# Performance work log

Measured on AMD Instinct MI355X. Metric: run time of the kernel, lower is better.

## Reference

```python
import jax, jax.numpy as jnp
import numpy as np

ALPHA = 0.2  # leaky relu slope
NEG = -9e15  # mask fill value from the torch code


def gat_layer(x, adj_mask, W, a):
    """One dense GAT attention head.
    Equivalent math to the torch layer, without materializing the
    [N, N, 2F] a_input tensor: a^T [h_i ; h_j] = (h @ a1)_i + (h @ a2)_j.
    x: [N, Fin], adj_mask: [N, N] bool, W: [Fin, Fout], a: [2*Fout, 1].
    """
    h = x @ W                              # [N, Fout]
    Fo = W.shape[1]
    s_src = h @ a[:Fo, 0]                  # [N]
    s_dst = h @ a[Fo:, 0]                  # [N]
    e = jax.nn.leaky_relu(s_src[:, None] + s_dst[None, :], ALPHA)  # [N, N]
    e = jnp.where(adj_mask, e, NEG)
    attn = jax.nn.softmax(e, axis=1)       # dropout is a no-op in eval mode
    return attn @ h                        # [N, Fout]


def setup_inputs() -> dict:
    key = jax.random.key(0)
    ks = jax.random.split(key, 6)
    N, nfeat, nhid, nclass, nheads = 4096, 512, 64, 32, 8
    x = jax.random.normal(ks[0], (N, nfeat), dtype=jnp.float32)
    adj = jax.random.randint(ks[1], (N, N), 0, 2, dtype=jnp.int32)
    # params scaled like torch uniform(-1/sqrt(fan_in), 1/sqrt(fan_in))
    W_att = jax.random.normal(ks[2], (nheads, nfeat, nhid), dtype=jnp.float32) / np.sqrt(nfeat)
    a_att = jax.random.normal(ks[3], (nheads, 2 * nhid, 1), dtype=jnp.float32) / np.sqrt(2 * nhid)
    W_out = jax.random.normal(ks[4], (nhid * nheads, nclass), dtype=jnp.float32) / np.sqrt(nhid * nheads)
    a_out = jax.random.normal(ks[5], (2 * nclass, 1), dtype=jnp.float32) / np.sqrt(2 * nclass)
    return {"x": x, "adj": adj, "W_att": W_att, "a_att": a_att,
            "W_out": W_out, "a_out": a_out}


def reference(x, adj, W_att, a_att, W_out, a_out):
    adj_mask = adj > 0  # [N, N]
    # multi-head layer, concat=True => elu per head, concat along features
    heads = jax.vmap(lambda W, a: jax.nn.elu(gat_layer(x, adj_mask, W, a)))(W_att, a_att)  # [H, N, nhid]
    H, N, Fh = heads.shape
    hcat = jnp.transpose(heads, (1, 0, 2)).reshape(N, H * Fh)  # [N, H*nhid]
    # output layer, concat=False, then elu applied by GAT.forward
    out = jax.nn.elu(gat_layer(hcat, adj_mask, W_out, a_out))  # [N, nclass]
    return out
```

## Files before the change

### kernel.cpp

```cpp
#include <hip/hip_runtime.h>
#include <math.h>

#define NN 4096
#define CC 512
#define MB (1024*1024)
#define LOG2E 1.4426950408889634f

typedef __attribute__((ext_vector_type(8))) __bf16 bf16x8;
typedef __attribute__((ext_vector_type(4))) float f32x4;
typedef unsigned short ushort_t;
typedef unsigned int uint_t;
typedef unsigned char uchar_t;

#if __has_builtin(__builtin_amdgcn_exp2f)
#define EXP2(x) __builtin_amdgcn_exp2f(x)
#else
#define EXP2(x) exp2f(x)
#endif

static __device__ __forceinline__ float elu1(float x){ return x > 0.f ? x : (__expf(x)-1.f); }
static __device__ __forceinline__ ushort_t f2bf(float f){
    union { float f; uint_t u; } v; v.f = f;
    uint_t r = (v.u + 0x7FFFu + ((v.u >> 16) & 1u)) >> 16;
    return (ushort_t)r;
}
static __device__ __forceinline__ float bf2f(ushort_t h){
    union { uint_t u; float f; } q; q.u = ((uint_t)h) << 16; return q.f;
}

__global__ void k_prepW(const float* __restrict__ Watt,
                        ushort_t* __restrict__ Wh, ushort_t* __restrict__ Wl){
    int idx = blockIdx.x*256 + threadIdx.x;
    int c = idx >> 7, kq = idx & 127, k = kq*4;
    ushort4 h4, l4;
    float v[4];
    #pragma unroll
    for(int j=0;j<4;j++)
        v[j] = Watt[(c>>6)*(512*64) + (k+j)*64 + (c&63)];
    h4.x = f2bf(v[0]); h4.y = f2bf(v[1]); h4.z = f2bf(v[2]); h4.w = f2bf(v[3]);
    l4.x = f2bf(v[0]-bf2f(h4.x)); l4.y = f2bf(v[1]-bf2f(h4.y));
    l4.z = f2bf(v[2]-bf2f(h4.z)); l4.w = f2bf(v[3]-bf2f(h4.w));
    *(ushort4*)&Wh[(size_t)c*512 + k] = h4;
    *(ushort4*)&Wl[(size_t)c*512 + k] = l4;
}

__global__ void k_splitx(const float* __restrict__ x,
                         ushort_t* __restrict__ xh, ushort_t* __restrict__ xl){
    int idx = blockIdx.x*256 + threadIdx.x;
    float4 v = *(const float4*)&x[(size_t)idx*4];
    ushort4 h4, l4;
    h4.x = f2bf(v.x); h4.y = f2bf(v.y); h4.z = f2bf(v.z); h4.w = f2bf(v.w);
    l4.x = f2bf(v.x-bf2f(h4.x)); l4.y = f2bf(v.y-bf2f(h4.y));
    l4.z = f2bf(v.z-bf2f(h4.z)); l4.w = f2bf(v.w-bf2f(h4.w));
    *(ushort4*)&xh[(size_t)idx*4] = h4;
    *(ushort4*)&xl[(size_t)idx*4] = l4;
}

__global__ void k_pack(const int* __restrict__ adj, uint_t* __restrict__ abits){
    int idx = blockIdx.x*256 + threadIdx.x;
    int i = idx >> 7, q = idx & 127;
    const int4* p = (const int4*)&adj[(size_t)i*NN + q*32];
    uint_t m = 0;
    #pragma unroll
    for(int g=0; g<8; g++){
        int4 v = p[g];
        m |= (uint_t)(v.x > 0) << (g*4 + 0);
        m |= (uint_t)(v.y > 0) << (g*4 + 1);
        m |= (uint_t)(v.z > 0) << (g*4 + 2);
        m |= (uint_t)(v.w > 0) << (g*4 + 3);
    }
    abits[idx] = m;
}

__global__ __launch_bounds__(256) void k_gemm1(
        const ushort_t* __restrict__ xh, const ushort_t* __restrict__ xl,
        const ushort_t* __restrict__ Wh, const ushort_t* __restrict__ Wl,
        const float* __restrict__ aatt,
        ushort_t* __restrict__ hT,
        float* __restrict__ ssrc2, float* __restrict__ sdst2){
    const int t = threadIdx.x;
    const int l = t & 63, wv = t >> 6;
    const int lr = l & 15, lg = l >> 4;
    const int ib = blockIdx.x*64 + wv*16;
    const int hd = blockIdx.y;
    const int j0 = hd*64;

    f32x4 acc[4] = {};
    #pragma unroll 2
    for(int ks=0; ks<16; ks++){
        const int kb = ks*32 + lg*8;
        bf16x8 ah = *(const bf16x8*)&xh[(size_t)(ib+lr)*512 + kb];
        bf16x8 al = *(const bf16x8*)&xl[(size_t)(ib+lr)*512 + kb];
        bf16x8 bh[4], bl[4];
        #pragma unroll
        for(int nt=0;nt<4;nt++){
            bh[nt] = *(const bf16x8*)&Wh[(size_t)(j0+nt*16+lr)*512 + kb];
            bl[nt] = *(const bf16x8*)&Wl[(size_t)(j0+nt*16+lr)*512 + kb];
        }
        #pragma unroll
        for(int nt=0;nt<4;nt++){
            acc[nt] = __builtin_amdgcn_mfma_f32_16x16x32_bf16(ah, bh[nt], acc[nt], 0,0,0);
            acc[nt] = __builtin_amdgcn_mfma_f32_16x16x32_bf16(al, bh[nt], acc[nt], 0,0,0);
            acc[nt] = __builtin_amdgcn_mfma_f32_16x16x32_bf16(ah, bl[nt], acc[nt], 0,0,0);
        }
    }
    #pragma unroll
    for(int nt=0;nt<4;nt++){
        const int col = j0 + nt*16 + lr;
        ushort4 o;
        o.x = f2bf(acc[nt][0]); o.y = f2bf(acc[nt][1]);
        o.z = f2bf(acc[nt][2]); o.w = f2bf(acc[nt][3]);
        *(ushort4*)&hT[(size_t)col*NN + ib + lg*4] = o;
    }
    float a1v[4], a2v[4];
    #pragma unroll
    for(int nt=0;nt<4;nt++){
        a1v[nt] = aatt[hd*128 + nt*16 + lr];
        a2v[nt] = aatt[hd*128 + 64 + nt*16 + lr];
    }
    #pragma unroll
    for(int r=0;r<4;r++){
        float ps = acc[0][r]*a1v[0] + acc[1][r]*a1v[1] + acc[2][r]*a1v[2] + acc[3][r]*a1v[3];
        float pd = acc[0][r]*a2v[0] + acc[1][r]*a2v[1] + acc[2][r]*a2v[2] + acc[3][r]*a2v[3];
        #pragma unroll
        for(int m=1;m<16;m<<=1){
            ps += __shfl_xor(ps, m);
            pd += __shfl_xor(pd, m);
        }
        if (lr == 0){
            ssrc2[hd*NN + ib + lg*4 + r] = ps*LOG2E;
            sdst2[hd*NN + ib + lg*4 + r] = pd*LOG2E;
        }
    }
}

__global__ __launch_bounds__(256) void k_attn1(
        const ushort_t* __restrict__ hT,
        const float* __restrict__ ssrc2, const float* __restrict__ sdst2,
        const uchar_t* __restrict__ abits,
        float* __restrict__ pnumT, float* __restrict__ pden){
    const int t = threadIdx.x;
    const int l = t & 63, wv = t >> 6;
    const int hd = blockIdx.z;
    const int i0 = blockIdx.x*64;
    const int jcc = blockIdx.y;
    const int lr = l & 15, lg = l >> 4;

    f32x4 acc[4][4] = {};
    f32x4 dacc[4] = {};

    float ss[4];
    #pragma unroll
    for(int mh=0;mh<4;mh++)
        ss[mh] = ssrc2[hd*NN + i0 + mh*16 + lr];

    bf16x8 ones;
    #pragma unroll
    for(int e=0;e<8;e++) ones[e] = (__bf16)1.0f;

    const int jwb = jcc*1024 + wv*256;
    const uchar_t* arow[4];
    #pragma unroll
    for(int mh=0;mh<4;mh++)
        arow[mh] = &abits[(size_t)(i0 + mh*16 + lr)*512 + (jwb >> 3)];

    bf16x8 bA[4], bB[4];
    float4 sdaA, sdbA, sdaB, sdbB;
    uint_t bitsA[4], bitsB[4];

#define LOAD1(SFX, JT) { \
    const int jb_ = jwb + (JT)*32 + lg*8; \
    _Pragma("unroll") \
    for(int nt=0;nt<4;nt++) \
        b##SFX[nt] = *(const bf16x8*)&hT[(size_t)(hd*64 + nt*16 + lr)*NN + jb_]; \
    sda##SFX = *(const float4*)&sdst2[hd*NN + jb_]; \
    sdb##SFX = *(const float4*)&sdst2[hd*NN + jb_ + 4]; \
    _Pragma("unroll") \
    for(int mh=0;mh<4;mh++) \
        bits##SFX[mh] = arow[mh][(JT)*4 + lg]; }

#define COMP1(SFX) { \
    float sdv[8] = {sda##SFX.x, sda##SFX.y, sda##SFX.z, sda##SFX.w, \
                    sdb##SFX.x, sdb##SFX.y, sdb##SFX.z, sdb##SFX.w}; \
    _Pragma("unroll") \
    for(int mh=0;mh<4;mh++){ \
        const uint_t bits = bits##SFX[mh]; \
        bf16x8 a; \
        _Pragma("unroll") \
        for(int e=0;e<8;e++){ \
            float s_ = ss[mh] + sdv[e]; \
            float t_ = fmaxf(s_, 0.2f*s_); \
            float w_ = EXP2(t_) * (float)((bits >> e) & 1u); \
            a[e] = (__bf16)w_; \
        } \
        _Pragma("unroll") \
        for(int nt=0;nt<4;nt++) \
            acc[mh][nt] = __builtin_amdgcn_mfma_f32_16x16x32_bf16( \
                a, b##SFX[nt], acc[mh][nt], 0, 0, 0); \
        dacc[mh] = __builtin_amdgcn_mfma_f32_16x16x32_bf16( \
                a, ones, dacc[mh], 0, 0, 0); \
    } }

    LOAD1(A, 0);
    for(int jt=0; jt<8; jt+=2){
        LOAD1(B, jt+1);
        COMP1(A);
        if (jt + 2 < 8) LOAD1(A, jt+2);
        COMP1(B);
    }
#undef LOAD1
#undef COMP1

    __shared__ f32x4 red[2][20][64];
    __syncthreads();
    if (wv >= 2){
        #pragma unroll
        for(int mh=0;mh<4;mh++){
            #pragma unroll
            for(int nt=0;nt<4;nt++) red[wv-2][mh*4+nt][l] = acc[mh][nt];
            red[wv-2][16+mh][l] = dacc[mh];
        }
    }
    __syncthreads();
    if (wv < 2){
        #pragma unroll
        for(int mh=0;mh<4;mh++){
            #pragma unroll
            for(int nt=0;nt<4;nt++) acc[mh][nt] += red[wv][mh*4+nt][l];
            dacc[mh] += red[wv][16+mh][l];
        }
    }
    __syncthreads();
    if (wv == 1){
        #pragma unroll
        for(int mh=0;mh<4;mh++){
            #pragma unroll
            for(int nt=0;nt<4;nt++) red[0][mh*4+nt][l] = acc[mh][nt];
            red[0][16+mh][l] = dacc[mh];
        }
    }
    __syncthreads();
    if (wv == 0){
        #pragma unroll
        for(int mh=0;mh<4;mh++){
            #pragma unroll
            for(int nt=0;nt<4;nt++){
                f32x4 v = acc[mh][nt] + red[0][mh*4+nt][l];
                int col = hd*64 + nt*16 + lr;
                float4 o = {v[0], v[1], v[2], v[3]};
                *(float4*)&pnumT[((size_t)jcc*512 + col)*NN + i0 + mh*16 + lg*4] = o;
            }
            f32x4 d = dacc[mh] + red[0][16+mh][l];
            if (lr == 0){
                #pragma unroll
                for(int r=0;r<4;r++)
                    pden[((size_t)jcc*8 + hd)*NN + i0 + mh*16 + lg*4 + r] = d[r];
            }
        }
    }
}

__global__ void k_reduce1T(const float* __restrict__ pnumT, const float* __restrict__ pden,
                           float* __restrict__ hcatT){
    int idx = blockIdx.x*256 + threadIdx.x;
    int c = idx >> 12, i = idx & 4095, hd = c >> 6;
    float s = 0.f, d = 0.f;
    #pragma unroll
    for(int jc=0;jc<4;jc++){
        s += pnumT[((size_t)jc*512 + c)*NN + i];
        d += pden[((size_t)jc*8 + hd)*NN + i];
    }
    hcatT[(size_t)c*NN + i] = elu1(s/d);
}

__global__ __launch_bounds__(256) void k_gemm2(const float* __restrict__ AT,
                                               const float* __restrict__ B,
                                               const float* __restrict__ aout,
                                               ushort_t* __restrict__ h2T,
                                               float* __restrict__ ss2,
                                               float* __restrict__ sd2){
    __shared__ float As[32][32];
    __shared__ float Bs[32][32];
    const int t = threadIdx.x;
    const int i0 = blockIdx.x*32;
    const int ty = t >> 4, tx = t & 15;
    float acc[2][2] = {{0.f,0.f},{0.f,0.f}};
    for(int k0=0;k0<512;k0+=32){
        __syncthreads();
        { int k = t >> 3, i4 = (t & 7)*4;
          *(float4*)&As[k][i4] = *(const float4*)&AT[(size_t)(k0+k)*NN + i0 + i4]; }
        { int k = t >> 3, n4 = (t & 7)*4;
          *(float4*)&Bs[k][n4] = *(const float4*)&B[(size_t)(k0+k)*32 + n4]; }
        __syncthreads();
        #pragma unroll
        for(int k=0;k<32;k++){
            float2 a2 = *(const float2*)&As[k][ty*2];
            float2 b2 = *(const float2*)&Bs[k][tx*2];
            acc[0][0] += a2.x*b2.x; acc[0][1] += a2.x*b2.y;
            acc[1][0] += a2.y*b2.x; acc[1][1] += a2.y*b2.y;
        }
    }
    #pragma unroll
    for(int a=0;a<2;a++){
        #pragma unroll
        for(int b=0;b<2;b++)
            h2T[(size_t)(tx*2+b)*NN + i0 + ty*2 + a] = f2bf(acc[a][b]);
    }
    float a1x = aout[tx*2], a1y = aout[tx*2+1];
    float a2x = aout[32+tx*2], a2y = aout[32+tx*2+1];
    #pragma unroll
    for(int a=0;a<2;a++){
        float ps = acc[a][0]*a1x + acc[a][1]*a1y;
        float pd = acc[a][0]*a2x + acc[a][1]*a2y;
        #pragma unroll
        for(int m=1;m<16;m<<=1){
            ps += __shfl_xor(ps, m);
            pd += __shfl_xor(pd, m);
        }
        if (tx == 0){
            ss2[i0 + ty*2 + a] = ps*LOG2E;
            sd2[i0 + ty*2 + a] = pd*LOG2E;
        }
    }
}

__global__ __launch_bounds__(256) void k_attn2(
        const ushort_t* __restrict__ h2T,
        const float* __restrict__ ss2, const float* __restrict__ sd2,
        const uchar_t* __restrict__ abits,
        float* __restrict__ pnum2T, float* __restrict__ pden2){
    const int t = threadIdx.x;
    const int l = t & 63, wv = t >> 6;
    const int i0 = blockIdx.x*64;
    const int jc = blockIdx.y;
    const int lr = l & 15, lg = l >> 4;

    f32x4 acc[4][2] = {};
    f32x4 dacc[4] = {};

    float ss[4];
    #pragma unroll
    for(int mh=0;mh<4;mh++)
        ss[mh] = ss2[i0 + mh*16 + lr];

    bf16x8 ones;
    #pragma unroll
    for(int e=0;e<8;e++) ones[e] = (__bf16)1.0f;

    const int jwb = jc*512 + wv*128;
    const uchar_t* arow[4];
    #pragma unroll
    for(int mh=0;mh<4;mh++)
        arow[mh] = &abits[(size_t)(i0 + mh*16 + lr)*512 + (jwb >> 3)];

    bf16x8 bA[2], bB[2];
    float4 sdaA, sdbA, sdaB, sdbB;
    uint_t bitsA[4], bitsB[4];

#define LOAD2(SFX, JT) { \
    const int jb_ = jwb + (JT)*32 + lg*8; \
    _Pragma("unroll") \
    for(int nt=0;nt<2;nt++) \
        b##SFX[nt] = *(const bf16x8*)&h2T[(size_t)(nt*16 + lr)*NN + jb_]; \
    sda##SFX = *(const float4*)&sd2[jb_]; \
    sdb##SFX = *(const float4*)&sd2[jb_ + 4]; \
    _Pragma("unroll") \
    for(int mh=0;mh<4;mh++) \
        bits##SFX[mh] = arow[mh][(JT)*4 + lg]; }

#define COMP2(SFX) { \
    float sdv[8] = {sda##SFX.x, sda##SFX.y, sda##SFX.z, sda##SFX.w, \
                    sdb##SFX.x, sdb##SFX.y, sdb##SFX.z, sdb##SFX.w}; \
    _Pragma("unroll") \
    for(int mh=0;mh<4;mh++){ \
        const uint_t bits = bits##SFX[mh]; \
        bf16x8 a; \
        _Pragma("unroll") \
        for(int e=0;e<8;e++){ \
            float s_ = ss[mh] + sdv[e]; \
            float t_ = fmaxf(s_, 0.2f*s_); \
            float w_ = EXP2(t_) * (float)((bits >> e) & 1u); \
            a[e] = (__bf16)w_; \
        } \
        _Pragma("unroll") \
        for(int nt=0;nt<2;nt++) \
            acc[mh][nt] = __builtin_amdgcn_mfma_f32_16x16x32_bf16( \
                a, b##SFX[nt], acc[mh][nt], 0, 0, 0); \
        dacc[mh] = __builtin_amdgcn_mfma_f32_16x16x32_bf16( \
                a, ones, dacc[mh], 0, 0, 0); \
    } }

    LOAD2(A, 0);
    for(int jt=0; jt<4; jt+=2){
        LOAD2(B, jt+1);
        COMP2(A);
        if (jt + 2 < 4) LOAD2(A, jt+2);
        COMP2(B);
    }
#undef LOAD2
#undef COMP2

    __shared__ f32x4 red2[2][12][64];
    __syncthreads();
    if (wv >= 2){
        #pragma unroll
        for(int mh=0;mh<4;mh++){
            #pragma unroll
            for(int nt=0;nt<2;nt++) red2[wv-2][mh*2+nt][l] = acc[mh][nt];
            red2[wv-2][8+mh][l] = dacc[mh];
        }
    }
    __syncthreads();
    if (wv < 2){
        #pragma unroll
        for(int mh=0;mh<4;mh++){
            #pragma unroll
            for(int nt=0;nt<2;nt++) acc[mh][nt] += red2[wv][mh*2+nt][l];
            dacc[mh] += red2[wv][8+mh][l];
        }
    }
    __syncthreads();
    if (wv == 1){
        #pragma unroll
        for(int mh=0;mh<4;mh++){
            #pragma unroll
            for(int nt=0;nt<2;nt++) red2[0][mh*2+nt][l] = acc[mh][nt];
            red2[0][8+mh][l] = dacc[mh];
        }
    }
    __syncthreads();
    if (wv == 0){
        #pragma unroll
        for(int mh=0;mh<4;mh++){
            #pragma unroll
            for(int nt=0;nt<2;nt++){
                f32x4 v = acc[mh][nt] + red2[0][mh*2+nt][l];
                int col = nt*16 + lr;
                float4 o = {v[0], v[1], v[2], v[3]};
                *(float4*)&pnum2T[((size_t)jc*32 + col)*NN + i0 + mh*16 + lg*4] = o;
            }
            f32x4 d = dacc[mh] + red2[0][8+mh][l];
            if (lr == 0){
                #pragma unroll
                for(int r=0;r<4;r++)
                    pden2[(size_t)jc*NN + i0 + mh*16 + lg*4 + r] = d[r];
            }
        }
    }
}

__global__ void k_reduce2(const float* __restrict__ pnum2T, const float* __restrict__ pden2,
                          float* __restrict__ out){
    int idx = blockIdx.x*256 + threadIdx.x;
    int c = idx >> 12, i = idx & 4095;
    float s = 0.f, d = 0.f;
    #pragma unroll
    for(int jc=0;jc<8;jc++){
        s += pnum2T[((size_t)jc*32 + c)*NN + i];
        d += pden2[(size_t)jc*NN + i];
    }
    out[(size_t)i*32 + c] = elu1(s/d);
}

extern "C" void kernel_launch(void* const* d_in, const int* in_sizes, int n_in,
                              void* d_out, int out_size, void* d_ws, size_t ws_size,
                              hipStream_t stream){
    const float* x    = (const float*)d_in[0];
    const int*   adj  = (const int*)  d_in[1];
    const float* Watt = (const float*)d_in[2];
    const float* aatt = (const float*)d_in[3];
    const float* Wout = (const float*)d_in[4];
    const float* aout = (const float*)d_in[5];
    float* out = (float*)d_out;
    char* ws = (char*)d_ws;

    float*    hcatT = (float*)   (ws + (size_t) 0*MB);
    ushort_t* Whi   = (ushort_t*)(ws + (size_t) 8*MB);
    ushort_t* Wlo   = (ushort_t*)(ws + (size_t) 8*MB + 512*1024);
    float*    ssrc2 = (float*)   (ws + (size_t) 9*MB);
    float*    sdst2 = (float*)   (ws + (size_t)10*MB);
    ushort_t* hT    = (ushort_t*)(ws + (size_t)11*MB);
    uint_t*   abits = (uint_t*)  (ws + (size_t)15*MB);
    float*    ss2   = (float*)   (ws + (size_t)18*MB);
    float*    sd2   = (float*)   (ws + (size_t)19*MB);
    ushort_t* h2T   = (ushort_t*)(ws + (size_t)20*MB);
    float*    pden  = (float*)   (ws + (size_t)21*MB);
    float*    pden2 = (float*)   (ws + (size_t)21*MB + 512*1024);
    float*    pnumT = (float*)   (ws + (size_t)22*MB);
    float*    pnum2T= pnumT;
    ushort_t* xh    = (ushort_t*)(ws + (size_t)46*MB);
    ushort_t* xl    = (ushort_t*)(ws + (size_t)50*MB);
    if (ws_size < (size_t)55*MB) return;

    k_prepW   <<<256, 256, 0, stream>>>(Watt, Whi, Wlo);
    k_splitx  <<<2048, 256, 0, stream>>>(x, xh, xl);
    k_pack    <<<2048, 256, 0, stream>>>(adj, abits);
    k_gemm1   <<<dim3(64,8), 256, 0, stream>>>(xh, xl, Whi, Wlo, aatt, hT, ssrc2, sdst2);
    k_attn1   <<<dim3(64,4,8), 256, 0, stream>>>(hT, ssrc2, sdst2, (const uchar_t*)abits, pnumT, pden);
    k_reduce1T<<<8192, 256, 0, stream>>>(pnumT, pden, hcatT);
    k_gemm2   <<<128, 256, 0, stream>>>(hcatT, Wout, aout, h2T, ss2, sd2);
    k_attn2   <<<dim3(64,8), 256, 0, stream>>>(h2T, ss2, sd2, (const uchar_t*)abits, pnum2T, pden2);
    k_reduce2 <<<512, 256, 0, stream>>>(pnum2T, pden2, out);
}
```

Baseline: 263.0 us.

## Fuse layer-1 split-K reduction into attention kernel and use MFMA for gemm2

The first attention kernel now runs 512 threads per block that cover the whole neighbour range. It reduces partial sums across waves in shared memory and writes the ELU-normalised hcat directly as split bf16 hi/lo arrays. This removes the partial-numerator buffer round trip and the separate reduce kernel. The second GEMM now uses bf16x3 MFMA on those arrays with a pre-transposed, pre-split Wout, and reduce2 is vectorised. The trade-off is fewer blocks in attn1 (512 instead of 2048) and a longer serial shared-memory reduction, plus scattered 2-byte stores of hcat.

```diff
diff --git a/kernel.cpp b/kernel.cpp
--- a/kernel.cpp
+++ b/kernel.cpp
@@ -28,20 +28,36 @@
     union { uint_t u; float f; } q; q.u = ((uint_t)h) << 16; return q.f;
 }
 
-__global__ void k_prepW(const float* __restrict__ Watt,
-                        ushort_t* __restrict__ Wh, ushort_t* __restrict__ Wl){
+__global__ void k_prep(const float* __restrict__ Watt, const float* __restrict__ Wout,
+                       ushort_t* __restrict__ Wh, ushort_t* __restrict__ Wl,
+                       ushort_t* __restrict__ Wth, ushort_t* __restrict__ Wtl){
     int idx = blockIdx.x*256 + threadIdx.x;
-    int c = idx >> 7, kq = idx & 127, k = kq*4;
-    ushort4 h4, l4;
-    float v[4];
-    #pragma unroll
-    for(int j=0;j<4;j++)
-        v[j] = Watt[(c>>6)*(512*64) + (k+j)*64 + (c&63)];
-    h4.x = f2bf(v[0]); h4.y = f2bf(v[1]); h4.z = f2bf(v[2]); h4.w = f2bf(v[3]);
-    l4.x = f2bf(v[0]-bf2f(h4.x)); l4.y = f2bf(v[1]-bf2f(h4.y));
-    l4.z = f2bf(v[2]-bf2f(h4.z)); l4.w = f2bf(v[3]-bf2f(h4.w));
-    *(ushort4*)&Wh[(size_t)c*512 + k] = h4;
-    *(ushort4*)&Wl[(size_t)c*512 + k] = l4;
+    if (idx < 512*128){
+        int c = idx >> 7, kq = idx & 127, k = kq*4;
+        ushort4 h4, l4;
+        float v[4];
+        #pragma unroll
+        for(int j=0;j<4;j++)
+            v[j] = Watt[(c>>6)*(512*64) + (k+j)*64 + (c&63)];
+        h4.x = f2bf(v[0]); h4.y = f2bf(v[1]); h4.z = f2bf(v[2]); h4.w = f2bf(v[3]);
+        l4.x = f2bf(v[0]-bf2f(h4.x)); l4.y = f2bf(v[1]-bf2f(h4.y));
+        l4.z = f2bf(v[2]-bf2f(h4.z)); l4.w = f2bf(v[3]-bf2f(h4.w));
+        *(ushort4*)&Wh[(size_t)c*512 + k] = h4;
+        *(ushort4*)&Wl[(size_t)c*512 + k] = l4;
+    } else if (idx < 512*128 + 32*128){
+        int idx2 = idx - 512*128;
+        int n = idx2 >> 7, kq = idx2 & 127, k = kq*4;
+        ushort4 h4, l4;
+        float v[4];
+        #pragma unroll
+        for(int j=0;j<4;j++)
+            v[j] = Wout[(size_t)(k+j)*32 + n];
+        h4.x = f2bf(v[0]); h4.y = f2bf(v[1]); h4.z = f2bf(v[2]); h4.w = f2bf(v[3]);
+        l4.x = f2bf(v[0]-bf2f(h4.x)); l4.y = f2bf(v[1]-bf2f(h4.y));
+        l4.z = f2bf(v[2]-bf2f(h4.z)); l4.w = f2bf(v[3]-bf2f(h4.w));
+        *(ushort4*)&Wth[(size_t)n*512 + k] = h4;
+        *(ushort4*)&Wtl[(size_t)n*512 + k] = l4;
+    }
 }
 
 __global__ void k_splitx(const float* __restrict__ x,
@@ -134,16 +150,15 @@
     }
 }
 
-__global__ __launch_bounds__(256) void k_attn1(
+__global__ __launch_bounds__(512, 4) void k_attn1(
         const ushort_t* __restrict__ hT,
         const float* __restrict__ ssrc2, const float* __restrict__ sdst2,
         const uchar_t* __restrict__ abits,
-        float* __restrict__ pnumT, float* __restrict__ pden){
+        ushort_t* __restrict__ hch, ushort_t* __restrict__ hcl){
     const int t = threadIdx.x;
     const int l = t & 63, wv = t >> 6;
-    const int hd = blockIdx.z;
+    const int hd = blockIdx.y;
     const int i0 = blockIdx.x*64;
-    const int jcc = blockIdx.y;
     const int lr = l & 15, lg = l >> 4;
 
     f32x4 acc[4][4] = {};
@@ -158,7 +173,7 @@
     #pragma unroll
     for(int e=0;e<8;e++) ones[e] = (__bf16)1.0f;
 
-    const int jwb = jcc*1024 + wv*256;
+    const int jwb = wv*512;
     const uchar_t* arow[4];
     #pragma unroll
     for(int mh=0;mh<4;mh++)
@@ -202,124 +217,143 @@
     } }
 
     LOAD1(A, 0);
-    for(int jt=0; jt<8; jt+=2){
+    for(int jt=0; jt<16; jt+=2){
         LOAD1(B, jt+1);
         COMP1(A);
-        if (jt + 2 < 8) LOAD1(A, jt+2);
+        if (jt + 2 < 16) LOAD1(A, jt+2);
         COMP1(B);
     }
 #undef LOAD1
 #undef COMP1
 
-    __shared__ f32x4 red[2][20][64];
-    __syncthreads();
-    if (wv >= 2){
-        #pragma unroll
-        for(int mh=0;mh<4;mh++){
-            #pragma unroll
-            for(int nt=0;nt<4;nt++) red[wv-2][mh*4+nt][l] = acc[mh][nt];
-            red[wv-2][16+mh][l] = dacc[mh];
-        }
-    }
-    __syncthreads();
-    if (wv < 2){
-        #pragma unroll
-        for(int mh=0;mh<4;mh++){
-            #pragma unroll
-            for(int nt=0;nt<4;nt++) acc[mh][nt] += red[wv][mh*4+nt][l];
-            dacc[mh] += red[wv][16+mh][l];
-        }
-    }
-    __syncthreads();
-    if (wv == 1){
-        #pragma unroll
-        for(int mh=0;mh<4;mh++){
-            #pragma unroll
-            for(int nt=0;nt<4;nt++) red[0][mh*4+nt][l] = acc[mh][nt];
-            red[0][16+mh][l] = dacc[mh];
-        }
-    }
-    __syncthreads();
-    if (wv == 0){
-        #pragma unroll
-        for(int mh=0;mh<4;mh++){
-            #pragma unroll
-            for(int nt=0;nt<4;nt++){
-                f32x4 v = acc[mh][nt] + red[0][mh*4+nt][l];
-                int col = hd*64 + nt*16 + lr;
-                float4 o = {v[0], v[1], v[2], v[3]};
-                *(float4*)&pnumT[((size_t)jcc*512 + col)*NN + i0 + mh*16 + lg*4] = o;
-            }
-            f32x4 d = dacc[mh] + red[0][16+mh][l];
-            if (lr == 0){
-                #pragma unroll
-                for(int r=0;r<4;r++)
-                    pden[((size_t)jcc*8 + hd)*NN + i0 + mh*16 + lg*4 + r] = d[r];
-            }
-        }
-    }
-}
-
-__global__ void k_reduce1T(const float* __restrict__ pnumT, const float* __restrict__ pden,
-                           float* __restrict__ hcatT){
-    int idx = blockIdx.x*256 + threadIdx.x;
-    int c = idx >> 12, i = idx & 4095, hd = c >> 6;
-    float s = 0.f, d = 0.f;
-    #pragma unroll
-    for(int jc=0;jc<4;jc++){
-        s += pnumT[((size_t)jc*512 + c)*NN + i];
-        d += pden[((size_t)jc*8 + hd)*NN + i];
-    }
-    hcatT[(size_t)c*NN + i] = elu1(s/d);
-}
-
-__global__ __launch_bounds__(256) void k_gemm2(const float* __restrict__ AT,
-                                               const float* __restrict__ B,
-                                               const float* __restrict__ aout,
-                                               ushort_t* __restrict__ h2T,
-                                               float* __restrict__ ss2,
-                                               float* __restrict__ sd2){
-    __shared__ float As[32][32];
-    __shared__ float Bs[32][32];
+    __shared__ f32x4 red[4][10][64];
+
+#define CHUNK_REDUCE(M0) { \
+    __syncthreads(); \
+    if (wv >= 4){ \
+        _Pragma("unroll") \
+        for(int m=0;m<2;m++){ \
+            _Pragma("unroll") \
+            for(int nt=0;nt<4;nt++) red[wv-4][m*4+nt][l] = acc[(M0)+m][nt]; \
+            red[wv-4][8+m][l] = dacc[(M0)+m]; \
+        } \
+    } \
+    __syncthreads(); \
+    if (wv < 4){ \
+        _Pragma("unroll") \
+        for(int m=0;m<2;m++){ \
+            _Pragma("unroll") \
+            for(int nt=0;nt<4;nt++) acc[(M0)+m][nt] += red[wv][m*4+nt][l]; \
+            dacc[(M0)+m] += red[wv][8+m][l]; \
+        } \
+    } \
+    __syncthreads(); \
+    if (wv == 2 || wv == 3){ \
+        _Pragma("unroll") \
+        for(int m=0;m<2;m++){ \
+            _Pragma("unroll") \
+            for(int nt=0;nt<4;nt++) red[wv-2][m*4+nt][l] = acc[(M0)+m][nt]; \
+            red[wv-2][8+m][l] = dacc[(M0)+m]; \
+        } \
+    } \
+    __syncthreads(); \
+    if (wv < 2){ \
+        _Pragma("unroll") \
+        for(int m=0;m<2;m++){ \
+            _Pragma("unroll") \
+            for(int nt=0;nt<4;nt++) acc[(M0)+m][nt] += red[wv][m*4+nt][l]; \
+            dacc[(M0)+m] += red[wv][8+m][l]; \
+        } \
+    } \
+    __syncthreads(); \
+    if (wv == 1){ \
+        _Pragma("unroll") \
+        for(int m=0;m<2;m++){ \
+            _Pragma("unroll") \
+            for(int nt=0;nt<4;nt++) red[0][m*4+nt][l] = acc[(M0)+m][nt]; \
+            red[0][8+m][l] = dacc[(M0)+m]; \
+        } \
+    } \
+    __syncthreads(); \
+    if (wv == 0){ \
+        _Pragma("unroll") \
+        for(int m=0;m<2;m++){ \
+            const int mh = (M0)+m; \
+            _Pragma("unroll") \
+            for(int nt=0;nt<4;nt++) acc[mh][nt] += red[0][m*4+nt][l]; \
+            dacc[mh] += red[0][8+m][l]; \
+            _Pragma("unroll") \
+            for(int nt=0;nt<4;nt++){ \
+                const int col = hd*64 + nt*16 + lr; \
+                _Pragma("unroll") \
+                for(int r=0;r<4;r++){ \
+                    const int row = i0 + mh*16 + lg*4 + r; \
+                    float v_ = elu1(acc[mh][nt][r] / dacc[mh][r]); \
+                    ushort_t hi_ = f2bf(v_); \
+                    hch[(size_t)row*512 + col] = hi_; \
+                    hcl[(size_t)row*512 + col] = f2bf(v_ - bf2f(hi_)); \
+                } \
+            } \
+        } \
+    } }
+
+    CHUNK_REDUCE(0);
+    CHUNK_REDUCE(2);
+#undef CHUNK_REDUCE
+}
+
+__global__ __launch_bounds__(256) void k_gemm2(
+        const ushort_t* __restrict__ hch, const ushort_t* __restrict__ hcl,
+        const ushort_t* __restrict__ Wth, const ushort_t* __restrict__ Wtl,
+        const float* __restrict__ aout,
+        ushort_t* __restrict__ h2T, float* __restrict__ ss2, float* __restrict__ sd2){
     const int t = threadIdx.x;
-    const int i0 = blockIdx.x*32;
-    const int ty = t >> 4, tx = t & 15;
-    float acc[2][2] = {{0.f,0.f},{0.f,0.f}};
-    for(int k0=0;k0<512;k0+=32){
-        __syncthreads();
-        { int k = t >> 3, i4 = (t & 7)*4;
-          *(float4*)&As[k][i4] = *(const float4*)&AT[(size_t)(k0+k)*NN + i0 + i4]; }
-        { int k = t >> 3, n4 = (t & 7)*4;
-          *(float4*)&Bs[k][n4] = *(const float4*)&B[(size_t)(k0+k)*32 + n4]; }
-        __syncthreads();
-        #pragma unroll
-        for(int k=0;k<32;k++){
-            float2 a2 = *(const float2*)&As[k][ty*2];
-            float2 b2 = *(const float2*)&Bs[k][tx*2];
-            acc[0][0] += a2.x*b2.x; acc[0][1] += a2.x*b2.y;
-            acc[1][0] += a2.y*b2.x; acc[1][1] += a2.y*b2.y;
-        }
-    }
-    #pragma unroll
-    for(int a=0;a<2;a++){
-        #pragma unroll
-        for(int b=0;b<2;b++)
-            h2T[(size_t)(tx*2+b)*NN + i0 + ty*2 + a] = f2bf(acc[a][b]);
-    }
-    float a1x = aout[tx*2], a1y = aout[tx*2+1];
-    float a2x = aout[32+tx*2], a2y = aout[32+tx*2+1];
-    #pragma unroll
-    for(int a=0;a<2;a++){
-        float ps = acc[a][0]*a1x + acc[a][1]*a1y;
-        float pd = acc[a][0]*a2x + acc[a][1]*a2y;
+    const int l = t & 63, wv = t >> 6;
+    const int lr = l & 15, lg = l >> 4;
+    const int ib = blockIdx.x*64 + wv*16;
+
+    f32x4 acc[2] = {};
+    #pragma unroll 2
+    for(int ks=0; ks<16; ks++){
+        const int kb = ks*32 + lg*8;
+        bf16x8 ah = *(const bf16x8*)&hch[(size_t)(ib+lr)*512 + kb];
+        bf16x8 al = *(const bf16x8*)&hcl[(size_t)(ib+lr)*512 + kb];
+        bf16x8 bh[2], bl[2];
+        #pragma unroll
+        for(int nt=0;nt<2;nt++){
+            bh[nt] = *(const bf16x8*)&Wth[(size_t)(nt*16+lr)*512 + kb];
+            bl[nt] = *(const bf16x8*)&Wtl[(size_t)(nt*16+lr)*512 + kb];
+        }
+        #pragma unroll
+        for(int nt=0;nt<2;nt++){
+            acc[nt] = __builtin_amdgcn_mfma_f32_16x16x32_bf16(ah, bh[nt], acc[nt], 0,0,0);
+            acc[nt] = __builtin_amdgcn_mfma_f32_16x16x32_bf16(al, bh[nt], acc[nt], 0,0,0);
+            acc[nt] = __builtin_amdgcn_mfma_f32_16x16x32_bf16(ah, bl[nt], acc[nt], 0,0,0);
+        }
+    }
+    #pragma unroll
+    for(int nt=0;nt<2;nt++)
+        #pragma unroll
+        for(int r=0;r<4;r++)
+            h2T[(size_t)(nt*16+lr)*NN + ib + lg*4 + r] = f2bf(acc[nt][r]);
+    float a1v[2], a2v[2];
+    #pragma unroll
+    for(int nt=0;nt<2;nt++){
+        a1v[nt] = aout[nt*16 + lr];
+        a2v[nt] = aout[32 + nt*16 + lr];
+    }
+    #pragma unroll
+    for(int r=0;r<4;r++){
+        float ps = acc[0][r]*a1v[0] + acc[1][r]*a1v[1];
+        float pd = acc[0][r]*a2v[0] + acc[1][r]*a2v[1];
         #pragma unroll
         for(int m=1;m<16;m<<=1){
             ps += __shfl_xor(ps, m);
             pd += __shfl_xor(pd, m);
         }
-        if (tx == 0){
-            ss2[i0 + ty*2 + a] = ps*LOG2E;
-            sd2[i0 + ty*2 + a] = pd*LOG2E;
+        if (lr == 0){
+            ss2[ib + lg*4 + r] = ps*LOG2E;
+            sd2[ib + lg*4 + r] = pd*LOG2E;
         }
     }
 }
@@ -452,14 +486,16 @@
 __global__ void k_reduce2(const float* __restrict__ pnum2T, const float* __restrict__ pden2,
                           float* __restrict__ out){
     int idx = blockIdx.x*256 + threadIdx.x;
-    int c = idx >> 12, i = idx & 4095;
-    float s = 0.f, d = 0.f;
+    int c = idx >> 10, i4 = (idx & 1023)*4;
+    f32x4 s = {}, d = {};
     #pragma unroll
     for(int jc=0;jc<8;jc++){
-        s += pnum2T[((size_t)jc*32 + c)*NN + i];
-        d += pden2[(size_t)jc*NN + i];
-    }
-    out[(size_t)i*32 + c] = elu1(s/d);
+        s += *(const f32x4*)&pnum2T[((size_t)jc*32 + c)*NN + i4];
+        d += *(const f32x4*)&pden2[(size_t)jc*NN + i4];
+    }
+    #pragma unroll
+    for(int r=0;r<4;r++)
+        out[(size_t)(i4+r)*32 + c] = elu1(s[r]/d[r]);
 }
 
 extern "C" void kernel_launch(void* const* d_in, const int* in_sizes, int n_in,
@@ -474,31 +510,31 @@
     float* out = (float*)d_out;
     char* ws = (char*)d_ws;
 
-    float*    hcatT = (float*)   (ws + (size_t) 0*MB);
+    ushort_t* hch   = (ushort_t*)(ws + (size_t) 0*MB);
+    ushort_t* hcl   = (ushort_t*)(ws + (size_t) 4*MB);
     ushort_t* Whi   = (ushort_t*)(ws + (size_t) 8*MB);
     ushort_t* Wlo   = (ushort_t*)(ws + (size_t) 8*MB + 512*1024);
     float*    ssrc2 = (float*)   (ws + (size_t) 9*MB);
     float*    sdst2 = (float*)   (ws + (size_t)10*MB);
     ushort_t* hT    = (ushort_t*)(ws + (size_t)11*MB);
     uint_t*   abits = (uint_t*)  (ws + (size_t)15*MB);
+    ushort_t* Wth   = (ushort_t*)(ws + (size_t)17*MB);
+    ushort_t* Wtl   = (ushort_t*)(ws + (size_t)17*MB + 64*1024);
     float*    ss2   = (float*)   (ws + (size_t)18*MB);
     float*    sd2   = (float*)   (ws + (size_t)19*MB);
     ushort_t* h2T   = (ushort_t*)(ws + (size_t)20*MB);
-    float*    pden  = (float*)   (ws + (size_t)21*MB);
-    float*    pden2 = (float*)   (ws + (size_t)21*MB + 512*1024);
-    float*    pnumT = (float*)   (ws + (size_t)22*MB);
-    float*    pnum2T= pnumT;
-    ushort_t* xh    = (ushort_t*)(ws + (size_t)46*MB);
-    ushort_t* xl    = (ushort_t*)(ws + (size_t)50*MB);
-    if (ws_size < (size_t)55*MB) return;
-
-    k_prepW   <<<256, 256, 0, stream>>>(Watt, Whi, Wlo);
+    float*    pden2 = (float*)   (ws + (size_t)21*MB);
+    float*    pnum2T= (float*)   (ws + (size_t)22*MB);
+    ushort_t* xh    = (ushort_t*)(ws + (size_t)26*MB);
+    ushort_t* xl    = (ushort_t*)(ws + (size_t)30*MB);
+    if (ws_size < (size_t)40*MB) return;
+
+    k_prep    <<<272, 256, 0, stream>>>(Watt, Wout, Whi, Wlo, Wth, Wtl);
     k_splitx  <<<2048, 256, 0, stream>>>(x, xh, xl);
     k_pack    <<<2048, 256, 0, stream>>>(adj, abits);
     k_gemm1   <<<dim3(64,8), 256, 0, stream>>>(xh, xl, Whi, Wlo, aatt, hT, ssrc2, sdst2);
-    k_attn1   <<<dim3(64,4,8), 256, 0, stream>>>(hT, ssrc2, sdst2, (const uchar_t*)abits, pnumT, pden);
-    k_reduce1T<<<8192, 256, 0, stream>>>(pnumT, pden, hcatT);
-    k_gemm2   <<<128, 256, 0, stream>>>(hcatT, Wout, aout, h2T, ss2, sd2);
+    k_attn1   <<<dim3(64,8), 512, 0, stream>>>(hT, ssrc2, sdst2, (const uchar_t*)abits, hch, hcl);
+    k_gemm2   <<<64, 256, 0, stream>>>(hch, hcl, Wth, Wtl, aout, h2T, ss2, sd2);
     k_attn2   <<<dim3(64,8), 256, 0, stream>>>(h2T, ss2, sd2, (const uchar_t*)abits, pnum2T, pden2);
-    k_reduce2 <<<512, 256, 0, stream>>>(pnum2T, pden2, out);
-}
+    k_reduce2 <<<128, 256, 0, stream>>>(pnum2T, pden2, out);
+}
```

New measurement: 409.0 us. +55.5%, slower.
